# Kernel optimization log

Measured on AMD Instinct MI355X. Metric: run time of the kernel, lower is better.

## Reference

```python
import jax, jax.numpy as jnp
import numpy as np

G = 128      # voxel grid extent per axis
N = 300000   # number of occupied input voxels
CIN = 32
COUT = 64

_FILTER = np.array([[-1, -1, -1], [-1, -1, 0], [-1, 0, -1], [-1, 0, 0],
                    [0, -1, -1], [0, -1, 0], [0, 0, -1], [0, 0, 0]], dtype=np.int64)


def calculate_grid(in_pos):
    # faithful numpy port of the torch calculate_grid (returns even integer coords;
    # the actual out position is coord + 0.5)
    out = (in_pos[:, None, :].astype(np.int64) + _FILTER[None, :, :]).reshape(-1, 3)
    out = out[out.min(axis=1) >= 0]
    out = out[~((out % 2).astype(bool).any(axis=1))]
    out = np.unique(out, axis=0)
    return out  # [M, 3] even ints


def setup_inputs() -> dict:
    key = jax.random.key(0)
    k1, k2 = jax.random.split(key)
    rng = np.random.default_rng(0)
    lin = rng.choice(G ** 3, size=N, replace=False)  # unique voxel coords
    pos = np.stack(np.unravel_index(lin, (G, G, G)), axis=1).astype(np.int32)
    features = jax.random.normal(k1, (N, CIN), dtype=jnp.float32)
    weight = jax.random.normal(k2, (2, 2, 2, CIN, COUT), dtype=jnp.float32) * 0.05
    return {"features": features, "in_positions": jnp.asarray(pos), "weight": weight}


def reference(features, in_positions, weight):
    pos = np.asarray(in_positions)            # concrete int coords (constants)
    out_int = calculate_grid(pos)             # [M, 3] even ints; out pos = out_int + 0.5

    # dense voxel-hash: grid cell -> input row index (-1 = empty)
    p = jnp.asarray(pos)
    idx_grid = jnp.full((G, G, G), -1, dtype=jnp.int32)
    idx_grid = idx_grid.at[p[:, 0], p[:, 1], p[:, 2]].set(
        jnp.arange(p.shape[0], dtype=jnp.int32))

    # 2x2x2 kernel, offset=-0.5: kernel index per axis = in_coord - even_out_coord in {0,1}
    offsets = np.stack(np.meshgrid(np.arange(2), np.arange(2), np.arange(2),
                                   indexing='ij'), axis=-1).reshape(8, 3)
    nbs = jnp.asarray(out_int[None, :, :] + offsets[:, None, :])   # [8, M, 3]
    idx = idx_grid[nbs[..., 0], nbs[..., 1], nbs[..., 2]]          # [8, M]
    valid = idx >= 0
    gathered = jnp.where(valid[..., None],
                         features[jnp.maximum(idx, 0)], 0.0)       # [8, M, CIN]
    w = weight.reshape(8, CIN, COUT)
    out_feat = jnp.einsum('kmc,kcf->mf', gathered, w)              # [M, COUT]

    out_positions = (jnp.asarray(out_int, dtype=jnp.float32) + 0.5) / 2.0
    return out_feat, out_positions
```

## Files before the change

kernel.cpp:

```cpp
#include <hip/hip_runtime.h>

#define GFINE 128
#define GC 64
#define NCELLS (GC * GC * GC)
#define CIN 32
#define COUT 64

typedef __attribute__((ext_vector_type(8))) short bf16x8;
typedef __attribute__((ext_vector_type(4))) float f32x4;

__device__ __forceinline__ short f2bf(float f) {
    union { float f; unsigned u; } v; v.f = f;
    unsigned r = v.u + 0x7fffu + ((v.u >> 16) & 1u);
    return (short)(r >> 16);
}

__global__ void scatter_kernel(const int* __restrict__ pos, int n,
                               int* __restrict__ idx_grid, int* __restrict__ flags) {
    int i = blockIdx.x * blockDim.x + threadIdx.x;
    if (i >= n) return;
    int x = pos[i * 3 + 0];
    int y = pos[i * 3 + 1];
    int z = pos[i * 3 + 2];
    idx_grid[(x * GFINE + y) * GFINE + z] = i;
    flags[((x >> 1) * GC + (y >> 1)) * GC + (z >> 1)] = 1;
}

__global__ void scan1_kernel(const int* __restrict__ flags, int* __restrict__ scan,
                             int* __restrict__ blockSums) {
    __shared__ int lds[256];
    int tid = threadIdx.x, bid = blockIdx.x;
    int4 v = ((const int4*)flags)[bid * 256 + tid];
    int s = v.x + v.y + v.z + v.w;
    lds[tid] = s;
    __syncthreads();
    for (int off = 1; off < 256; off <<= 1) {
        int t = (tid >= off) ? lds[tid - off] : 0;
        __syncthreads();
        lds[tid] += t;
        __syncthreads();
    }
    int incl = lds[tid];
    int excl = incl - s;
    int4 o;
    o.x = excl;
    o.y = excl + v.x;
    o.z = excl + v.x + v.y;
    o.w = excl + v.x + v.y + v.z;
    ((int4*)scan)[bid * 256 + tid] = o;
    if (tid == 255) blockSums[bid] = incl;
}

__global__ void scan2_kernel(int* __restrict__ blockSums) {
    __shared__ int lds[256];
    int tid = threadIdx.x;
    int s = blockSums[tid];
    lds[tid] = s;
    __syncthreads();
    for (int off = 1; off < 256; off <<= 1) {
        int t = (tid >= off) ? lds[tid - off] : 0;
        __syncthreads();
        lds[tid] += t;
        __syncthreads();
    }
    blockSums[tid] = lds[tid] - s;
}

__global__ void compact_kernel(const int* __restrict__ flags, const int* __restrict__ scan,
                               const int* __restrict__ blockSums,
                               int* __restrict__ cellList, float* __restrict__ out_pos) {
    int cell = blockIdx.x * blockDim.x + threadIdx.x;
    if (cell >= NCELLS) return;
    if (!flags[cell]) return;
    int m = scan[cell] + blockSums[cell >> 10];
    cellList[m] = cell;
    int cx = cell >> 12, cy = (cell >> 6) & 63, cz = cell & 63;
    out_pos[m * 3 + 0] = cx + 0.25f;
    out_pos[m * 3 + 1] = cy + 0.25f;
    out_pos[m * 3 + 2] = cz + 0.25f;
}

__global__ void wswz_kernel(const float* __restrict__ w, short* __restrict__ wswz) {
    int t = blockIdx.x * blockDim.x + threadIdx.x;
    int lane = t & 63, cb = (t >> 6) & 3, k = t >> 8;
    bf16x8 o;
#pragma unroll
    for (int e = 0; e < 8; ++e)
        o[e] = f2bf(w[(k * CIN + ((lane >> 4) * 8 + e)) * COUT + cb * 16 + (lane & 15)]);
    ((bf16x8*)wswz)[t] = o;
}

__global__ __launch_bounds__(256) void conv6_kernel(
    const float* __restrict__ feat, const short* __restrict__ wswz,
    const int* __restrict__ idx_grid, const int* __restrict__ cellList,
    int M, float* __restrict__ out_feat) {
    const int lane = threadIdx.x & 63;
    const int wv = threadIdx.x >> 6;
    const int base = (blockIdx.x * 4 + wv) * 16;
    if (base >= M) return;
    const int cslot = lane & 15;
    const int tgrp  = lane >> 4;

    int rank = base + cslot;
    if (rank >= M) rank = M - 1;
    int cell = cellList[rank];
    int cx = cell >> 12, cy = (cell >> 6) & 63, cz = cell & 63;
    int vfb = ((cx * 2) * GFINE + cy * 2) * GFINE + cz * 2;

    int toff = ((tgrp >> 1) & 1) * GFINE + (tgrp & 1);
    int tA = idx_grid[vfb + toff];
    int tB = idx_grid[vfb + GFINE * GFINE + toff];

    float4 u[8], v[8];
    int rr[8];
#pragma unroll
    for (int k = 0; k < 8; ++k) {
        int r = __shfl(k < 4 ? tA : tB, cslot + ((k & 3) << 4), 64);
        rr[k] = r;
        if (r >= 0) {
            const float4* fr = (const float4*)(feat + (size_t)r * CIN + tgrp * 8);
            u[k] = fr[0];
            v[k] = fr[1];
        }
    }

    const bf16x8* wf = (const bf16x8*)wswz;
    f32x4 acc0 = {0.f, 0.f, 0.f, 0.f}, acc1 = acc0, acc2 = acc0, acc3 = acc0;
#pragma unroll
    for (int k = 0; k < 8; ++k) {
        bf16x8 a = {0, 0, 0, 0, 0, 0, 0, 0};
        if (rr[k] >= 0) {
            a[0] = f2bf(u[k].x); a[1] = f2bf(u[k].y);
            a[2] = f2bf(u[k].z); a[3] = f2bf(u[k].w);
            a[4] = f2bf(v[k].x); a[5] = f2bf(v[k].y);
            a[6] = f2bf(v[k].z); a[7] = f2bf(v[k].w);
        }
        acc0 = __builtin_amdgcn_mfma_f32_16x16x32_bf16(a, wf[(k * 4 + 0) * 64 + lane], acc0, 0, 0, 0);
        acc1 = __builtin_amdgcn_mfma_f32_16x16x32_bf16(a, wf[(k * 4 + 1) * 64 + lane], acc1, 0, 0, 0);
        acc2 = __builtin_amdgcn_mfma_f32_16x16x32_bf16(a, wf[(k * 4 + 2) * 64 + lane], acc2, 0, 0, 0);
        acc3 = __builtin_amdgcn_mfma_f32_16x16x32_bf16(a, wf[(k * 4 + 3) * 64 + lane], acc3, 0, 0, 0);
    }

#pragma unroll
    for (int i = 0; i < 4; ++i) {
        int row = base + tgrp * 4 + i;
        if (row < M) {
            float* o = out_feat + (size_t)row * COUT + cslot;
            o[0]  = acc0[i];
            o[16] = acc1[i];
            o[32] = acc2[i];
            o[48] = acc3[i];
        }
    }
}

extern "C" void kernel_launch(void* const* d_in, const int* in_sizes, int n_in,
                              void* d_out, int out_size, void* d_ws, size_t ws_size,
                              hipStream_t stream) {
    const float* feat   = (const float*)d_in[0];
    const int*   pos    = (const int*)d_in[1];
    const float* weight = (const float*)d_in[2];
    int n = in_sizes[1] / 3;
    int M = out_size / 67;

    char* ws = (char*)d_ws;
    int*   idx_grid  = (int*)(ws);
    int*   flags     = (int*)(ws + (size_t)8388608);
    int*   scan      = (int*)(ws + (size_t)9437184);
    int*   blockSums = (int*)(ws + (size_t)10485760);
    int*   cellList  = (int*)(ws + (size_t)10489856);
    short* wswz      = (short*)(ws + (size_t)11538432);

    hipMemsetAsync(idx_grid, 0xFF, (size_t)GFINE * GFINE * GFINE * 4, stream);
    hipMemsetAsync(flags, 0, (size_t)NCELLS * 4, stream);

    scatter_kernel<<<(n + 255) / 256, 256, 0, stream>>>(pos, n, idx_grid, flags);
    wswz_kernel<<<8, 256, 0, stream>>>(weight, wswz);
    scan1_kernel<<<256, 256, 0, stream>>>(flags, scan, blockSums);
    scan2_kernel<<<1, 256, 0, stream>>>(blockSums);

    float* out_feat = (float*)d_out;
    float* out_pos  = (float*)d_out + (size_t)M * COUT;
    compact_kernel<<<NCELLS / 256, 256, 0, stream>>>(flags, scan, blockSums,
                                                     cellList, out_pos);

    conv6_kernel<<<(M + 63) / 64, 256, 0, stream>>>(feat, wswz, idx_grid,
                                                    cellList, M, out_feat);
}
```

Measured before the change: 57.69 us.

## Use cell-major neighbor table with occupancy bitmask and single-pass decoupled-lookback scan

Reorders the voxel hash so each coarse cell's 8 children sit contiguously, with an atomicOr occupancy bitmask per cell. This removes the 8MB memset of the index grid, because validity now comes from the bitmask rather than -1 sentinels. The three scan and compact kernels are merged into one kernel using decoupled lookback, and the weight swizzle and zeroing are folded into a setup kernel, which cuts launches and intermediate buffers. The conv kernel reads the 8 neighbor indices with two int4 loads instead of strided grid reads plus shuffles. The trade-offs are atomics in scatter and a spin-wait lookback that assumes blocks make forward progress in order.

```diff
diff --git a/kernel.cpp b/kernel.cpp
--- a/kernel.cpp
+++ b/kernel.cpp
@@ -15,23 +15,54 @@
     return (short)(r >> 16);
 }
 
+#define TAB_OFF   0u
+#define OCC_OFF   8388608u
+#define CL_OFF    9437184u
+#define ST_OFF    10485760u
+#define WSWZ_OFF  10489856u
+
+__global__ void setup_kernel(const float* __restrict__ w, char* __restrict__ ws) {
+    int bid = blockIdx.x, tid = threadIdx.x;
+    if (bid < 256) {
+        ((int4*)(ws + OCC_OFF))[bid * 256 + tid] = make_int4(0, 0, 0, 0);
+    } else if (bid == 256) {
+        if (tid < 128) ((int4*)(ws + ST_OFF))[tid] = make_int4(0, 0, 0, 0);
+    } else {
+        int t = (bid - 257) * 256 + tid;
+        int lane = t & 63, cb = (t >> 6) & 3, k = t >> 8;
+        bf16x8 o;
+#pragma unroll
+        for (int e = 0; e < 8; ++e)
+            o[e] = f2bf(w[(k * CIN + ((lane >> 4) * 8 + e)) * COUT + cb * 16 + (lane & 15)]);
+        ((bf16x8*)(ws + WSWZ_OFF))[t] = o;
+    }
+}
+
 __global__ void scatter_kernel(const int* __restrict__ pos, int n,
-                               int* __restrict__ idx_grid, int* __restrict__ flags) {
+                               int* __restrict__ tab, int* __restrict__ occ) {
     int i = blockIdx.x * blockDim.x + threadIdx.x;
     if (i >= n) return;
     int x = pos[i * 3 + 0];
     int y = pos[i * 3 + 1];
     int z = pos[i * 3 + 2];
-    idx_grid[(x * GFINE + y) * GFINE + z] = i;
-    flags[((x >> 1) * GC + (y >> 1)) * GC + (z >> 1)] = 1;
-}
-
-__global__ void scan1_kernel(const int* __restrict__ flags, int* __restrict__ scan,
-                             int* __restrict__ blockSums) {
+    int cell = ((x >> 1) * GC + (y >> 1)) * GC + (z >> 1);
+    int k = ((x & 1) << 2) | ((y & 1) << 1) | (z & 1);
+    tab[cell * 8 + k] = i;
+    atomicOr(&occ[cell], 1 << k);
+}
+
+#define FLAG_AGG (1ull << 62)
+#define FLAG_PFX (2ull << 62)
+#define VAL_MASK ((1ull << 62) - 1)
+__global__ __launch_bounds__(256) void scan_compact_kernel(
+    const int* __restrict__ occ, unsigned long long* __restrict__ state,
+    int* __restrict__ cellList, float* __restrict__ out_pos) {
     __shared__ int lds[256];
+    __shared__ int excl_sh;
     int tid = threadIdx.x, bid = blockIdx.x;
-    int4 v = ((const int4*)flags)[bid * 256 + tid];
-    int s = v.x + v.y + v.z + v.w;
+    int4 o = ((const int4*)occ)[bid * 256 + tid];
+    int c0 = (o.x != 0), c1 = (o.y != 0), c2 = (o.z != 0), c3 = (o.w != 0);
+    int s = c0 + c1 + c2 + c3;
     lds[tid] = s;
     __syncthreads();
     for (int off = 1; off < 256; off <<= 1) {
@@ -40,59 +71,50 @@
         lds[tid] += t;
         __syncthreads();
     }
-    int incl = lds[tid];
-    int excl = incl - s;
-    int4 o;
-    o.x = excl;
-    o.y = excl + v.x;
-    o.z = excl + v.x + v.y;
-    o.w = excl + v.x + v.y + v.z;
-    ((int4*)scan)[bid * 256 + tid] = o;
-    if (tid == 255) blockSums[bid] = incl;
-}
-
-__global__ void scan2_kernel(int* __restrict__ blockSums) {
-    __shared__ int lds[256];
-    int tid = threadIdx.x;
-    int s = blockSums[tid];
-    lds[tid] = s;
+    if (tid == 255) {
+        unsigned long long agg = (unsigned long long)lds[255];
+        if (bid == 0) {
+            __hip_atomic_store(&state[0], FLAG_PFX | agg, __ATOMIC_RELEASE,
+                               __HIP_MEMORY_SCOPE_AGENT);
+            excl_sh = 0;
+        } else {
+            __hip_atomic_store(&state[bid], FLAG_AGG | agg, __ATOMIC_RELEASE,
+                               __HIP_MEMORY_SCOPE_AGENT);
+            unsigned long long run = 0;
+            int j = bid - 1;
+            while (true) {
+                unsigned long long sv = __hip_atomic_load(&state[j], __ATOMIC_ACQUIRE,
+                                                          __HIP_MEMORY_SCOPE_AGENT);
+                unsigned long long f = sv >> 62;
+                if (f == 2) { run += sv & VAL_MASK; break; }
+                if (f == 1) { run += sv & VAL_MASK; --j; }
+            }
+            __hip_atomic_store(&state[bid], FLAG_PFX | (run + agg), __ATOMIC_RELEASE,
+                               __HIP_MEMORY_SCOPE_AGENT);
+            excl_sh = (int)run;
+        }
+    }
     __syncthreads();
-    for (int off = 1; off < 256; off <<= 1) {
-        int t = (tid >= off) ? lds[tid - off] : 0;
-        __syncthreads();
-        lds[tid] += t;
-        __syncthreads();
-    }
-    blockSums[tid] = lds[tid] - s;
-}
-
-__global__ void compact_kernel(const int* __restrict__ flags, const int* __restrict__ scan,
-                               const int* __restrict__ blockSums,
-                               int* __restrict__ cellList, float* __restrict__ out_pos) {
-    int cell = blockIdx.x * blockDim.x + threadIdx.x;
-    if (cell >= NCELLS) return;
-    if (!flags[cell]) return;
-    int m = scan[cell] + blockSums[cell >> 10];
-    cellList[m] = cell;
-    int cx = cell >> 12, cy = (cell >> 6) & 63, cz = cell & 63;
-    out_pos[m * 3 + 0] = cx + 0.25f;
-    out_pos[m * 3 + 1] = cy + 0.25f;
-    out_pos[m * 3 + 2] = cz + 0.25f;
-}
-
-__global__ void wswz_kernel(const float* __restrict__ w, short* __restrict__ wswz) {
-    int t = blockIdx.x * blockDim.x + threadIdx.x;
-    int lane = t & 63, cb = (t >> 6) & 3, k = t >> 8;
-    bf16x8 o;
-#pragma unroll
-    for (int e = 0; e < 8; ++e)
-        o[e] = f2bf(w[(k * CIN + ((lane >> 4) * 8 + e)) * COUT + cb * 16 + (lane & 15)]);
-    ((bf16x8*)wswz)[t] = o;
-}
-
-__global__ __launch_bounds__(256) void conv6_kernel(
+    int rank = excl_sh + lds[tid] - s;
+    int cellBase = (bid * 256 + tid) * 4;
+    int oc[4] = {o.x, o.y, o.z, o.w};
+#pragma unroll
+    for (int c = 0; c < 4; ++c) {
+        if (oc[c]) {
+            int cell = cellBase + c;
+            cellList[rank] = cell | (oc[c] << 18);
+            int cx = cell >> 12, cy = (cell >> 6) & 63, cz = cell & 63;
+            out_pos[rank * 3 + 0] = cx + 0.25f;
+            out_pos[rank * 3 + 1] = cy + 0.25f;
+            out_pos[rank * 3 + 2] = cz + 0.25f;
+            ++rank;
+        }
+    }
+}
+
+__global__ __launch_bounds__(256) void conv_kernel(
     const float* __restrict__ feat, const short* __restrict__ wswz,
-    const int* __restrict__ idx_grid, const int* __restrict__ cellList,
+    const int* __restrict__ tab, const int* __restrict__ cellList,
     int M, float* __restrict__ out_feat) {
     const int lane = threadIdx.x & 63;
     const int wv = threadIdx.x >> 6;
@@ -103,22 +125,19 @@
 
     int rank = base + cslot;
     if (rank >= M) rank = M - 1;
-    int cell = cellList[rank];
-    int cx = cell >> 12, cy = (cell >> 6) & 63, cz = cell & 63;
-    int vfb = ((cx * 2) * GFINE + cy * 2) * GFINE + cz * 2;
-
-    int toff = ((tgrp >> 1) & 1) * GFINE + (tgrp & 1);
-    int tA = idx_grid[vfb + toff];
-    int tB = idx_grid[vfb + GFINE * GFINE + toff];
+    int e = cellList[rank];
+    int cell = e & 0x3FFFF;
+    int occ8 = (e >> 18) & 0xFF;
+
+    const int4* tp = (const int4*)(tab + cell * 8);
+    int4 t0 = tp[0], t1 = tp[1];
+    int rr[8] = {t0.x, t0.y, t0.z, t0.w, t1.x, t1.y, t1.z, t1.w};
 
     float4 u[8], v[8];
-    int rr[8];
 #pragma unroll
     for (int k = 0; k < 8; ++k) {
-        int r = __shfl(k < 4 ? tA : tB, cslot + ((k & 3) << 4), 64);
-        rr[k] = r;
-        if (r >= 0) {
-            const float4* fr = (const float4*)(feat + (size_t)r * CIN + tgrp * 8);
+        if ((occ8 >> k) & 1) {
+            const float4* fr = (const float4*)(feat + (size_t)rr[k] * CIN + tgrp * 8);
             u[k] = fr[0];
             v[k] = fr[1];
         }
@@ -129,7 +148,7 @@
 #pragma unroll
     for (int k = 0; k < 8; ++k) {
         bf16x8 a = {0, 0, 0, 0, 0, 0, 0, 0};
-        if (rr[k] >= 0) {
+        if ((occ8 >> k) & 1) {
             a[0] = f2bf(u[k].x); a[1] = f2bf(u[k].y);
             a[2] = f2bf(u[k].z); a[3] = f2bf(u[k].w);
             a[4] = f2bf(v[k].x); a[5] = f2bf(v[k].y);
@@ -164,26 +183,18 @@
     int M = out_size / 67;
 
     char* ws = (char*)d_ws;
-    int*   idx_grid  = (int*)(ws);
-    int*   flags     = (int*)(ws + (size_t)8388608);
-    int*   scan      = (int*)(ws + (size_t)9437184);
-    int*   blockSums = (int*)(ws + (size_t)10485760);
-    int*   cellList  = (int*)(ws + (size_t)10489856);
-    short* wswz      = (short*)(ws + (size_t)11538432);
-
-    hipMemsetAsync(idx_grid, 0xFF, (size_t)GFINE * GFINE * GFINE * 4, stream);
-    hipMemsetAsync(flags, 0, (size_t)NCELLS * 4, stream);
-
-    scatter_kernel<<<(n + 255) / 256, 256, 0, stream>>>(pos, n, idx_grid, flags);
-    wswz_kernel<<<8, 256, 0, stream>>>(weight, wswz);
-    scan1_kernel<<<256, 256, 0, stream>>>(flags, scan, blockSums);
-    scan2_kernel<<<1, 256, 0, stream>>>(blockSums);
+    int* tab                   = (int*)(ws + TAB_OFF);
+    int* occ                   = (int*)(ws + OCC_OFF);
+    int* cellList              = (int*)(ws + CL_OFF);
+    unsigned long long* state  = (unsigned long long*)(ws + ST_OFF);
+    short* wswz                = (short*)(ws + WSWZ_OFF);
 
     float* out_feat = (float*)d_out;
     float* out_pos  = (float*)d_out + (size_t)M * COUT;
-    compact_kernel<<<NCELLS / 256, 256, 0, stream>>>(flags, scan, blockSums,
-                                                     cellList, out_pos);
-
-    conv6_kernel<<<(M + 63) / 64, 256, 0, stream>>>(feat, wswz, idx_grid,
-                                                    cellList, M, out_feat);
-}
+
+    setup_kernel<<<265, 256, 0, stream>>>(weight, ws);
+    scatter_kernel<<<(n + 255) / 256, 256, 0, stream>>>(pos, n, tab, occ);
+    scan_compact_kernel<<<256, 256, 0, stream>>>(occ, state, cellList, out_pos);
+    conv_kernel<<<(M + 63) / 64, 256, 0, stream>>>(feat, wswz, tab, cellList,
+                                                   M, out_feat);
+}
```

New measurement: 109.7 us. 90.1% more time.
